# Kernel optimization log

Measured on AMD Instinct MI355X. Metric: run time of the kernel, lower is better.

## Reference

```python
import jax, jax.numpy as jnp
import numpy as np

DT, TAU = 1.0, 10.0
C1 = np.float32(1.0 - DT / TAU)  # 0.9
C2 = np.float32(DT / TAU)        # 0.1
EPS = 1e-5
NOISE_STD = 0.1


def setup_inputs() -> dict:
    key = jax.random.key(0)
    ks = jax.random.split(key, 5)
    B, T, I, H, O = 256, 2000, 4, 100, 1
    x = jax.random.normal(ks[0], (B, T, I), dtype=jnp.float32)
    W_in = jax.random.normal(ks[1], (I, H), dtype=jnp.float32)
    W_hidden = jax.random.normal(ks[2], (H, H), dtype=jnp.float32) / np.sqrt(H)
    sigma = jax.random.normal(ks[3], (B, T, H), dtype=jnp.float32) * NOISE_STD
    gamma = jnp.ones((H,), dtype=jnp.float32)
    beta = jnp.zeros((H,), dtype=jnp.float32)
    fc_w = jax.random.normal(ks[4], (O, H), dtype=jnp.float32) / np.sqrt(H)
    fc_b = jnp.zeros((O,), dtype=jnp.float32)
    return {"x": x, "W_in": W_in, "W_hidden": W_hidden, "sigma": sigma,
            "gamma": gamma, "beta": beta, "fc_w": fc_w, "fc_b": fc_b}


def _rnn_scan(x, W_in, W_hidden, sigma):
    B = x.shape[0]
    H = W_hidden.shape[0]
    w_input = jnp.einsum('bti,ih->bth', x, W_in)  # [B,T,H]
    h0 = jnp.zeros((B, H), dtype=x.dtype)

    def step(h, inp):
        w_t, s_t = inp  # each [B,H]
        h_new = C1 * h + C2 * (w_t + jnp.tanh(h) @ W_hidden) + s_t
        return h_new, h_new

    h_last, ys = jax.lax.scan(step,
                              h0,
                              (jnp.swapaxes(w_input, 0, 1), jnp.swapaxes(sigma, 0, 1)))
    out = jnp.swapaxes(ys, 0, 1)  # [B,T,H]
    return out, h_last


def reference(x, W_in, W_hidden, sigma, gamma, beta, fc_w, fc_b):
    out, h_last = _rnn_scan(x, W_in, W_hidden, sigma)
    # BatchNorm1d (training mode): per-channel stats over batch and time, biased var
    mean = jnp.mean(out, axis=(0, 1))
    var = jnp.var(out, axis=(0, 1))
    out = (out - mean) * jax.lax.rsqrt(var + EPS) * gamma + beta
    out = jnp.tanh(out)
    out = out @ fc_w.T + fc_b  # [B,T,1]
    return out, h_last
```

## Files before the change

### kernel.cpp

```cpp
#include <hip/hip_runtime.h>
#include <hip/hip_fp16.h>

#define BB 256
#define TT 2000
#define HH 100
#define II 4
#define KP 28
#define CH 16
#define NCHUNK (TT / CH)

typedef __attribute__((ext_vector_type(8))) unsigned short ushort8_t;

static constexpr float kC1 = 0.9f;
static constexpr float kC2 = 0.1f;
static constexpr float kEPS = 1e-5f;

__device__ __forceinline__ float fast_tanh(float x) {
    const float xc = fminf(fmaxf(x, -15.f), 15.f);
    const float e  = __builtin_amdgcn_exp2f(xc * 2.88539008177793f);
    return (e - 1.f) * __builtin_amdgcn_rcpf(e + 1.f);
}

__global__ __launch_bounds__(512) void crnn_scan_kernel(
    const float* __restrict__ x, const float* __restrict__ Win,
    const float* __restrict__ Wh, const float* __restrict__ sigma,
    __half* __restrict__ out_buf, float* __restrict__ partials,
    float* __restrict__ d_out )
{
    const int b   = blockIdx.x;
    const int tid = threadIdx.x;
    const int j   = tid >> 2;
    const int kg  = tid & 3;
    const bool act = (j < HH);
    const int jc  = act ? j : (HH - 1);

    __shared__ float4 thb[2][4 * KP / 4];
    {
        float* ths = (float*)thb;
        for (int i = tid; i < 2 * 4 * KP; i += 512) ths[i] = 0.f;
    }

    const int k0 = kg * 25;
    auto ldw = [&](int i) -> float { return (i < 25) ? Wh[(k0 + i) * HH + jc] : 0.f; };
    const float4 wc0 = make_float4(ldw( 0), ldw( 1), ldw( 2), ldw( 3));
    const float4 wc1 = make_float4(ldw( 4), ldw( 5), ldw( 6), ldw( 7));
    const float4 wc2 = make_float4(ldw( 8), ldw( 9), ldw(10), ldw(11));
    const float4 wc3 = make_float4(ldw(12), ldw(13), ldw(14), ldw(15));
    const float4 wc4 = make_float4(ldw(16), ldw(17), ldw(18), ldw(19));
    const float4 wc5 = make_float4(ldw(20), ldw(21), ldw(22), ldw(23));
    const float4 wc6 = make_float4(ldw(24), 0.f, 0.f, 0.f);

    const float win0 = Win[0 * HH + jc];
    const float win1 = Win[1 * HH + jc];
    const float win2 = Win[2 * HH + jc];
    const float win3 = Win[3 * HH + jc];

    const float* sig = sigma + (size_t)b * TT * HH + jc;
    const float* xp  = x + (size_t)b * TT * II;
    __half* op = out_buf + ((size_t)b * HH + jc) * TT;
    const int wslot = (jc / 25) * KP + (jc % 25);

    float h = 0.f, bsum = 0.f, bsq = 0.f;

    float sA[CH], wA[CH], sB[CH], wB[CH];

    auto loadc = [&](int t0, float (&ss)[CH], float (&ww)[CH]) {
#pragma unroll
        for (int i = 0; i < CH; ++i) ss[i] = sig[(size_t)(t0 + i) * HH];
#pragma unroll
        for (int i = 0; i < CH; ++i) {
            const float4 xv = *(const float4*)(xp + (size_t)(t0 + i) * II);
            ww[i] = xv.x * win0 + xv.y * win1 + xv.z * win2 + xv.w * win3;
        }
    };

    auto run_chunk = [&](int t0, const float (&ss)[CH], const float (&ww)[CH]) {
        unsigned int hw[CH / 2];
#pragma unroll
        for (int i = 0; i < CH; ++i) {
            const float thj = fast_tanh(h);
            if (kg == 0 && act) ((float*)thb[i & 1])[wslot] = thj;
            asm volatile("s_waitcnt lgkmcnt(0)" ::: "memory");
            __builtin_amdgcn_s_barrier();
            asm volatile("" ::: "memory");

            const float4* tb = (const float4*)&thb[i & 1][kg * (KP / 4)];
            const float4 t0v = tb[0], t1v = tb[1], t2v = tb[2], t3v = tb[3];
            const float4 t4v = tb[4], t5v = tb[5], t6v = tb[6];
            float a0 = t0v.x * wc0.x, a1 = t0v.y * wc0.y;
            float a2 = t0v.z * wc0.z, a3 = t0v.w * wc0.w;
            a0 = fmaf(t1v.x, wc1.x, a0); a1 = fmaf(t1v.y, wc1.y, a1);
            a2 = fmaf(t1v.z, wc1.z, a2); a3 = fmaf(t1v.w, wc1.w, a3);
            a0 = fmaf(t2v.x, wc2.x, a0); a1 = fmaf(t2v.y, wc2.y, a1);
            a2 = fmaf(t2v.z, wc2.z, a2); a3 = fmaf(t2v.w, wc2.w, a3);
            a0 = fmaf(t3v.x, wc3.x, a0); a1 = fmaf(t3v.y, wc3.y, a1);
            a2 = fmaf(t3v.z, wc3.z, a2); a3 = fmaf(t3v.w, wc3.w, a3);
            a0 = fmaf(t4v.x, wc4.x, a0); a1 = fmaf(t4v.y, wc4.y, a1);
            a2 = fmaf(t4v.z, wc4.z, a2); a3 = fmaf(t4v.w, wc4.w, a3);
            a0 = fmaf(t5v.x, wc5.x, a0); a1 = fmaf(t5v.y, wc5.y, a1);
            a2 = fmaf(t5v.z, wc5.z, a2); a3 = fmaf(t5v.w, wc5.w, a3);
            a0 = fmaf(t6v.x, wc6.x, a0); a1 = fmaf(t6v.y, wc6.y, a1);
            a2 = fmaf(t6v.z, wc6.z, a2); a3 = fmaf(t6v.w, wc6.w, a3);
            float sum = (a0 + a1) + (a2 + a3);
            sum += __shfl_xor(sum, 1, 64);
            sum += __shfl_xor(sum, 2, 64);

            h = fmaf(kC1, h, kC2 * (ww[i] + sum)) + ss[i];

            const unsigned int hb = (unsigned int)__half_as_ushort(__float2half(h));
            if ((i & 1) == 0) hw[i >> 1] = hb; else hw[i >> 1] |= hb << 16;
            bsum += h;
            bsq = fmaf(h, h, bsq);
        }
        if (kg == 0 && act) {
            uint4* dst = (uint4*)(op + t0);
            dst[0] = make_uint4(hw[0], hw[1], hw[2], hw[3]);
            dst[1] = make_uint4(hw[4], hw[5], hw[6], hw[7]);
        }
    };

    __syncthreads();
    loadc(0, sA, wA);
    for (int c = 0; c < NCHUNK; ++c) {
        const int t0 = c * CH;
        if ((c & 1) == 0) {
            if (c + 1 < NCHUNK) loadc(t0 + CH, sB, wB);
            run_chunk(t0, sA, wA);
        } else {
            if (c + 1 < NCHUNK) loadc(t0 + CH, sA, wA);
            run_chunk(t0, sB, wB);
        }
    }

    if (kg == 0 && act) {
        partials[b * (2 * HH) + jc]      = bsum;
        partials[b * (2 * HH) + HH + jc] = bsq;
        d_out[(size_t)BB * TT + b * HH + jc] = h;
    }
}

__global__ __launch_bounds__(512) void crnn_bnstats_kernel(
    const float* __restrict__ partials, const float* __restrict__ gamma,
    const float* __restrict__ beta, float* __restrict__ scsh)
{
    const int tid = threadIdx.x;
    const int j = tid >> 2, c = tid & 3;
    if (j >= HH) return;
    float sum = 0.f, sq = 0.f;
    for (int b = c; b < BB; b += 4) {
        sum += partials[b * 2 * HH + j];
        sq  += partials[b * 2 * HH + HH + j];
    }
    sum += __shfl_xor(sum, 1, 64); sum += __shfl_xor(sum, 2, 64);
    sq  += __shfl_xor(sq,  1, 64); sq  += __shfl_xor(sq,  2, 64);
    if (c == 0) {
        const float invN = 1.f / (float)((long)BB * TT);
        const float mean = sum * invN;
        const float var  = sq * invN - mean * mean;
        const float sc   = gamma[j] * rsqrtf(var + kEPS);
        scsh[j]      = sc;
        scsh[HH + j] = fmaf(-mean, sc, beta[j]);
    }
}

__global__ __launch_bounds__(256) void crnn_out_kernel(
    const __half* __restrict__ buf, const float* __restrict__ scsh,
    const float* __restrict__ fcw, const float* __restrict__ fcb,
    float* __restrict__ out)
{
    const int b   = blockIdx.x;
    const int tid = threadIdx.x;
    const bool a  = (tid < TT / 8);
    const int t0  = tid * 8;
    const __half* bp = buf + (size_t)b * HH * TT + t0;
    const float bias = fcb[0];

    float acc[8] = {0.f, 0.f, 0.f, 0.f, 0.f, 0.f, 0.f, 0.f};
    for (int hh = 0; hh < HH; ++hh) {
        const float sc = scsh[hh], sh = scsh[HH + hh], fw = fcw[hh];
        if (a) {
            const ushort8_t v = *(const ushort8_t*)(bp + (size_t)hh * TT);
#pragma unroll
            for (int e = 0; e < 8; ++e) {
                const float vf = __half2float(__ushort_as_half((unsigned short)v[e]));
                acc[e] = fmaf(fast_tanh(fmaf(vf, sc, sh)), fw, acc[e]);
            }
        }
    }
    if (a) {
        float4* o = (float4*)(out + (size_t)b * TT + t0);
        o[0] = make_float4(acc[0] + bias, acc[1] + bias, acc[2] + bias, acc[3] + bias);
        o[1] = make_float4(acc[4] + bias, acc[5] + bias, acc[6] + bias, acc[7] + bias);
    }
}

extern "C" void kernel_launch(void* const* d_in, const int* in_sizes, int n_in,
                              void* d_out, int out_size, void* d_ws, size_t ws_size,
                              hipStream_t stream)
{
    const float* x     = (const float*)d_in[0];
    const float* Win   = (const float*)d_in[1];
    const float* Wh    = (const float*)d_in[2];
    const float* sigma = (const float*)d_in[3];
    const float* gamma = (const float*)d_in[4];
    const float* beta  = (const float*)d_in[5];
    const float* fcw   = (const float*)d_in[6];
    const float* fcb   = (const float*)d_in[7];
    float* out = (float*)d_out;

    char* ws = (char*)d_ws;
    __half* out_buf = (__half*)ws;
    float* partials = (float*)(ws + (size_t)BB * TT * HH * sizeof(__half));
    float* scsh     = (float*)((char*)partials + (size_t)BB * 2 * HH * sizeof(float));

    crnn_scan_kernel<<<BB, 512, 0, stream>>>(x, Win, Wh, sigma, out_buf, partials, out);
    crnn_bnstats_kernel<<<1, 512, 0, stream>>>(partials, gamma, beta, scsh);
    crnn_out_kernel<<<BB, 256, 0, stream>>>(out_buf, scsh, fcw, fcb, out);
}
```

Measured before the change: 1.083 ms.

## Use fp16 packed dot products with two hidden units per thread group in scan

The recurrent matvec is rewritten to hold W_hidden in packed fp16 and use v_dot2 (fdot2) instructions against a fp16 tanh(h) vector in shared memory. Each group of 4 threads now computes two output columns, which halves the block to 256 threads (4 waves) and shortens the barrier and LDS read path for each timestep. The chunk size drops to 8. This trades accuracy, since fp16 weights and activations are used in the recurrence, for fewer instructions and fewer waves synchronising on every serial step.

```diff
diff --git a/kernel.cpp b/kernel.cpp
--- a/kernel.cpp
+++ b/kernel.cpp
@@ -5,10 +5,12 @@
 #define TT 2000
 #define HH 100
 #define II 4
-#define KP 28
-#define CH 16
+#define CH 8
 #define NCHUNK (TT / CH)
-
+#define KSLOT 128
+
+typedef _Float16 half2v __attribute__((ext_vector_type(2)));
+typedef unsigned int uintv8 __attribute__((ext_vector_type(8)));
 typedef __attribute__((ext_vector_type(8))) unsigned short ushort8_t;
 
 static constexpr float kC1 = 0.9f;
@@ -21,7 +23,25 @@
     return (e - 1.f) * __builtin_amdgcn_rcpf(e + 1.f);
 }
 
-__global__ __launch_bounds__(512) void crnn_scan_kernel(
+__device__ __forceinline__ half2v u2h(unsigned int u) {
+    union { unsigned int u; half2v h; } c; c.u = u; return c.h;
+}
+__device__ __forceinline__ unsigned int pkh(float x, float y) {
+    union { half2v h; unsigned int u; } c;
+    c.h = half2v{(_Float16)x, (_Float16)y};
+    return c.u;
+}
+
+#if __has_builtin(__builtin_amdgcn_fdot2)
+#define DOT2(a, b, c) __builtin_amdgcn_fdot2((a), (b), (c), false)
+#else
+__device__ __forceinline__ float dot2_fb(half2v a, half2v b, float c) {
+    return fmaf((float)a.y, (float)b.y, fmaf((float)a.x, (float)b.x, c));
+}
+#define DOT2(a, b, c) dot2_fb((a), (b), (c))
+#endif
+
+__global__ __launch_bounds__(256) void crnn_scan_kernel(
     const float* __restrict__ x, const float* __restrict__ Win,
     const float* __restrict__ Wh, const float* __restrict__ sigma,
     __half* __restrict__ out_buf, float* __restrict__ partials,
@@ -29,39 +49,45 @@
 {
     const int b   = blockIdx.x;
     const int tid = threadIdx.x;
-    const int j   = tid >> 2;
+    const int p   = tid >> 2;
     const int kg  = tid & 3;
-    const bool act = (j < HH);
-    const int jc  = act ? j : (HH - 1);
-
-    __shared__ float4 thb[2][4 * KP / 4];
-    {
-        float* ths = (float*)thb;
-        for (int i = tid; i < 2 * 4 * KP; i += 512) ths[i] = 0.f;
-    }
-
-    const int k0 = kg * 25;
-    auto ldw = [&](int i) -> float { return (i < 25) ? Wh[(k0 + i) * HH + jc] : 0.f; };
-    const float4 wc0 = make_float4(ldw( 0), ldw( 1), ldw( 2), ldw( 3));
-    const float4 wc1 = make_float4(ldw( 4), ldw( 5), ldw( 6), ldw( 7));
-    const float4 wc2 = make_float4(ldw( 8), ldw( 9), ldw(10), ldw(11));
-    const float4 wc3 = make_float4(ldw(12), ldw(13), ldw(14), ldw(15));
-    const float4 wc4 = make_float4(ldw(16), ldw(17), ldw(18), ldw(19));
-    const float4 wc5 = make_float4(ldw(20), ldw(21), ldw(22), ldw(23));
-    const float4 wc6 = make_float4(ldw(24), 0.f, 0.f, 0.f);
-
-    const float win0 = Win[0 * HH + jc];
-    const float win1 = Win[1 * HH + jc];
-    const float win2 = Win[2 * HH + jc];
-    const float win3 = Win[3 * HH + jc];
-
-    const float* sig = sigma + (size_t)b * TT * HH + jc;
+    const bool act = (p < HH / 2);
+    const int pc  = act ? p : (HH / 2 - 1);
+    const int c0  = 2 * pc, c1 = 2 * pc + 1;
+    const int cs  = c0 + (kg & 1);
+    const bool wr = act && (kg < 2);
+
+    __shared__ unsigned int thb[2][KSLOT / 2];
+    for (int i = tid; i < KSLOT; i += 256) ((unsigned int*)thb)[i] = 0u;
+
+    const int k0 = kg * 32;
+    uintv8 wa0, wa1, wb0, wb1;
+#pragma unroll
+    for (int i = 0; i < 8; ++i) {
+        const int ka = k0 + 2 * i;
+        const int kb = k0 + 16 + 2 * i;
+        const float a0 = (ka < HH) ? Wh[(size_t)ka * HH + c0] : 0.f;
+        const float a1 = (ka + 1 < HH) ? Wh[(size_t)(ka + 1) * HH + c0] : 0.f;
+        const float a2 = (kb < HH) ? Wh[(size_t)kb * HH + c0] : 0.f;
+        const float a3 = (kb + 1 < HH) ? Wh[(size_t)(kb + 1) * HH + c0] : 0.f;
+        const float b0 = (ka < HH) ? Wh[(size_t)ka * HH + c1] : 0.f;
+        const float b1 = (ka + 1 < HH) ? Wh[(size_t)(ka + 1) * HH + c1] : 0.f;
+        const float b2 = (kb < HH) ? Wh[(size_t)kb * HH + c1] : 0.f;
+        const float b3 = (kb + 1 < HH) ? Wh[(size_t)(kb + 1) * HH + c1] : 0.f;
+        wa0[i] = pkh(a0, a1); wa1[i] = pkh(a2, a3);
+        wb0[i] = pkh(b0, b1); wb1[i] = pkh(b2, b3);
+    }
+
+    const float win0 = Win[0 * HH + cs];
+    const float win1 = Win[1 * HH + cs];
+    const float win2 = Win[2 * HH + cs];
+    const float win3 = Win[3 * HH + cs];
+
+    const float* sig = sigma + (size_t)b * TT * HH + cs;
     const float* xp  = x + (size_t)b * TT * II;
-    __half* op = out_buf + ((size_t)b * HH + jc) * TT;
-    const int wslot = (jc / 25) * KP + (jc % 25);
+    __half* op = out_buf + ((size_t)b * HH + cs) * TT;
 
     float h = 0.f, bsum = 0.f, bsq = 0.f;
-
     float sA[CH], wA[CH], sB[CH], wB[CH];
 
     auto loadc = [&](int t0, float (&ss)[CH], float (&ww)[CH]) {
@@ -78,45 +104,64 @@
         unsigned int hw[CH / 2];
 #pragma unroll
         for (int i = 0; i < CH; ++i) {
-            const float thj = fast_tanh(h);
-            if (kg == 0 && act) ((float*)thb[i & 1])[wslot] = thj;
+            const float thv = fast_tanh(h);
+            if (wr) ((unsigned short*)thb[i & 1])[cs] =
+                        (unsigned short)(pkh(thv, 0.f) & 0xffffu);
             asm volatile("s_waitcnt lgkmcnt(0)" ::: "memory");
             __builtin_amdgcn_s_barrier();
             asm volatile("" ::: "memory");
 
-            const float4* tb = (const float4*)&thb[i & 1][kg * (KP / 4)];
-            const float4 t0v = tb[0], t1v = tb[1], t2v = tb[2], t3v = tb[3];
-            const float4 t4v = tb[4], t5v = tb[5], t6v = tb[6];
-            float a0 = t0v.x * wc0.x, a1 = t0v.y * wc0.y;
-            float a2 = t0v.z * wc0.z, a3 = t0v.w * wc0.w;
-            a0 = fmaf(t1v.x, wc1.x, a0); a1 = fmaf(t1v.y, wc1.y, a1);
-            a2 = fmaf(t1v.z, wc1.z, a2); a3 = fmaf(t1v.w, wc1.w, a3);
-            a0 = fmaf(t2v.x, wc2.x, a0); a1 = fmaf(t2v.y, wc2.y, a1);
-            a2 = fmaf(t2v.z, wc2.z, a2); a3 = fmaf(t2v.w, wc2.w, a3);
-            a0 = fmaf(t3v.x, wc3.x, a0); a1 = fmaf(t3v.y, wc3.y, a1);
-            a2 = fmaf(t3v.z, wc3.z, a2); a3 = fmaf(t3v.w, wc3.w, a3);
-            a0 = fmaf(t4v.x, wc4.x, a0); a1 = fmaf(t4v.y, wc4.y, a1);
-            a2 = fmaf(t4v.z, wc4.z, a2); a3 = fmaf(t4v.w, wc4.w, a3);
-            a0 = fmaf(t5v.x, wc5.x, a0); a1 = fmaf(t5v.y, wc5.y, a1);
-            a2 = fmaf(t5v.z, wc5.z, a2); a3 = fmaf(t5v.w, wc5.w, a3);
-            a0 = fmaf(t6v.x, wc6.x, a0); a1 = fmaf(t6v.y, wc6.y, a1);
-            a2 = fmaf(t6v.z, wc6.z, a2); a3 = fmaf(t6v.w, wc6.w, a3);
-            float sum = (a0 + a1) + (a2 + a3);
-            sum += __shfl_xor(sum, 1, 64);
-            sum += __shfl_xor(sum, 2, 64);
-
-            h = fmaf(kC1, h, kC2 * (ww[i] + sum)) + ss[i];
-
-            const unsigned int hb = (unsigned int)__half_as_ushort(__float2half(h));
+            const uint4* tb = (const uint4*)thb[i & 1] + kg * 4;
+            const uint4 r0 = tb[0], r1 = tb[1], r2 = tb[2], r3 = tb[3];
+
+            float a0c, a1c, b0c, b1c;
+            a0c = DOT2(u2h(r0.x), u2h(wa0[0]), 0.f);
+            a1c = DOT2(u2h(r0.y), u2h(wa0[1]), 0.f);
+            b0c = DOT2(u2h(r0.x), u2h(wb0[0]), 0.f);
+            b1c = DOT2(u2h(r0.y), u2h(wb0[1]), 0.f);
+            a0c = DOT2(u2h(r0.z), u2h(wa0[2]), a0c);
+            a1c = DOT2(u2h(r0.w), u2h(wa0[3]), a1c);
+            b0c = DOT2(u2h(r0.z), u2h(wb0[2]), b0c);
+            b1c = DOT2(u2h(r0.w), u2h(wb0[3]), b1c);
+            a0c = DOT2(u2h(r1.x), u2h(wa0[4]), a0c);
+            a1c = DOT2(u2h(r1.y), u2h(wa0[5]), a1c);
+            b0c = DOT2(u2h(r1.x), u2h(wb0[4]), b0c);
+            b1c = DOT2(u2h(r1.y), u2h(wb0[5]), b1c);
+            a0c = DOT2(u2h(r1.z), u2h(wa0[6]), a0c);
+            a1c = DOT2(u2h(r1.w), u2h(wa0[7]), a1c);
+            b0c = DOT2(u2h(r1.z), u2h(wb0[6]), b0c);
+            b1c = DOT2(u2h(r1.w), u2h(wb0[7]), b1c);
+            a0c = DOT2(u2h(r2.x), u2h(wa1[0]), a0c);
+            a1c = DOT2(u2h(r2.y), u2h(wa1[1]), a1c);
+            b0c = DOT2(u2h(r2.x), u2h(wb1[0]), b0c);
+            b1c = DOT2(u2h(r2.y), u2h(wb1[1]), b1c);
+            a0c = DOT2(u2h(r2.z), u2h(wa1[2]), a0c);
+            a1c = DOT2(u2h(r2.w), u2h(wa1[3]), a1c);
+            b0c = DOT2(u2h(r2.z), u2h(wb1[2]), b0c);
+            b1c = DOT2(u2h(r2.w), u2h(wb1[3]), b1c);
+            a0c = DOT2(u2h(r3.x), u2h(wa1[4]), a0c);
+            a1c = DOT2(u2h(r3.y), u2h(wa1[5]), a1c);
+            b0c = DOT2(u2h(r3.x), u2h(wb1[4]), b0c);
+            b1c = DOT2(u2h(r3.y), u2h(wb1[5]), b1c);
+            a0c = DOT2(u2h(r3.z), u2h(wa1[6]), a0c);
+            a1c = DOT2(u2h(r3.w), u2h(wa1[7]), a1c);
+            b0c = DOT2(u2h(r3.z), u2h(wb1[6]), b0c);
+            b1c = DOT2(u2h(r3.w), u2h(wb1[7]), b1c);
+
+            float s0 = a0c + a1c;
+            float s1 = b0c + b1c;
+            s0 += __shfl_xor(s0, 1, 64); s0 += __shfl_xor(s0, 2, 64);
+            s1 += __shfl_xor(s1, 1, 64); s1 += __shfl_xor(s1, 2, 64);
+            const float ssel = (kg & 1) ? s1 : s0;
+
+            h = fmaf(kC1, h, kC2 * (ww[i] + ssel)) + ss[i];
+
+            const unsigned int hb = pkh(h, 0.f) & 0xffffu;
             if ((i & 1) == 0) hw[i >> 1] = hb; else hw[i >> 1] |= hb << 16;
             bsum += h;
             bsq = fmaf(h, h, bsq);
         }
-        if (kg == 0 && act) {
-            uint4* dst = (uint4*)(op + t0);
-            dst[0] = make_uint4(hw[0], hw[1], hw[2], hw[3]);
-            dst[1] = make_uint4(hw[4], hw[5], hw[6], hw[7]);
-        }
+        if (wr) *(uint4*)(op + t0) = make_uint4(hw[0], hw[1], hw[2], hw[3]);
     };
 
     __syncthreads();
@@ -132,10 +177,10 @@
         }
     }
 
-    if (kg == 0 && act) {
-        partials[b * (2 * HH) + jc]      = bsum;
-        partials[b * (2 * HH) + HH + jc] = bsq;
-        d_out[(size_t)BB * TT + b * HH + jc] = h;
+    if (wr) {
+        partials[b * (2 * HH) + cs]      = bsum;
+        partials[b * (2 * HH) + HH + cs] = bsq;
+        d_out[(size_t)BB * TT + b * HH + cs] = h;
     }
 }
 
@@ -213,7 +258,7 @@
     float* partials = (float*)(ws + (size_t)BB * TT * HH * sizeof(__half));
     float* scsh     = (float*)((char*)partials + (size_t)BB * 2 * HH * sizeof(float));
 
-    crnn_scan_kernel<<<BB, 512, 0, stream>>>(x, Win, Wh, sigma, out_buf, partials, out);
+    crnn_scan_kernel<<<BB, 256, 0, stream>>>(x, Win, Wh, sigma, out_buf, partials, out);
     crnn_bnstats_kernel<<<1, 512, 0, stream>>>(partials, gamma, beta, scsh);
     crnn_out_kernel<<<BB, 256, 0, stream>>>(out_buf, scsh, fcw, fcb, out);
 }
```

Measured after the change: 1.088 ms. About the same (+0.5%).
